# Performance work log

Measured on AMD Instinct MI355X. Metric: run time of the kernel, lower is better.

The kernel has to match this reference:

```python
import jax, jax.numpy as jnp
import numpy as np

K = 9      # kernel_size
H = 6      # num_head
HD = 64    # head_dim
D = H * HD # reduced_hidden_dim = 384
B, S = 16, 1024
OUT = 384  # hidden_dim // 2


def setup_inputs() -> dict:
    key = jax.random.key(0)
    k = jax.random.split(key, 5)
    q = jax.random.normal(k[0], (B, S, D), dtype=jnp.float32)
    ks = jax.random.normal(k[1], (B, S, D), dtype=jnp.float32)
    v = jax.random.normal(k[2], (B, S, D), dtype=jnp.float32)
    Wk = jax.random.normal(k[3], (K * H, D), dtype=jnp.float32) * 0.02
    bk = jnp.zeros((K * H,), dtype=jnp.float32)
    Wp = jax.random.normal(k[4], (OUT, D), dtype=jnp.float32) * 0.02
    bp = jnp.zeros((OUT,), dtype=jnp.float32)
    return {"q": q, "ks": ks, "v": v, "Wk": Wk, "bk": bk, "Wp": Wp, "bp": bp}


def reference(q, ks, v, Wk, bk, Wp, bp):
    b, s, d = v.shape
    pad = K // 2
    # expand4conv: zero-pad along seq and gather K-wide sliding windows
    vp = jnp.pad(v, ((0, 0), (pad, pad), (0, 0)))            # [B, S+K-1, D]
    win = jnp.stack([vp[:, i:i + s] for i in range(K)], -1)  # [B, S, D, K]
    win = win.reshape(b, s, H, HD, K)                        # [B, S, H, HD, K]
    # dynamic kernel: softmax over kernel taps
    logits = jnp.einsum('bsd,od->bso', q * ks, Wk) + bk       # [B, S, K*H]
    dk = jax.nn.softmax(logits.reshape(b, s, H, K), axis=-1)  # [B, S, H, K]
    # local weighted reduction over the window
    out = jnp.einsum('bshdk,bshk->bshd', win, dk).reshape(b, s, d)
    return jnp.einsum('bsd,od->bso', out, Wp) + bp            # [B, S, OUT]
```

## Files before the change

### kernel.cpp

```cpp
#include <hip/hip_runtime.h>
#include <hip/hip_bf16.h>

#define BB 16
#define SS 1024
#define DD 384
#define HH 6
#define KK 9
#define KH 54
#define OUTD 384
#define NKT 12
#define VLD 392
#define RPB 32
#define NTH 512

typedef __attribute__((ext_vector_type(4))) float floatx4;
typedef __attribute__((ext_vector_type(8))) __bf16 bf16x8;
typedef __attribute__((ext_vector_type(4))) __bf16 bf16x4;

__global__ __launch_bounds__(256) void cast_kernel(const float* __restrict__ Wk,
                                                   const float* __restrict__ Wp,
                                                   __bf16* __restrict__ WkT,
                                                   __bf16* __restrict__ WpT) {
    int i = blockIdx.x * 256 + threadIdx.x;
    if (i < 4 * NKT * 64 * 8) {
        int e = i & 7, lane = (i >> 3) & 63, t = i >> 9;
        int kstep = t % NKT, ntile = t / NKT;
        int row = ntile * 16 + (lane & 15);
        int col = kstep * 32 + ((lane >> 4) << 3) + e;
        WkT[i] = (row < KH) ? (__bf16)Wk[row * DD + col] : (__bf16)0.0f;
    } else if (i < 24576 + 24 * NKT * 64 * 8) {
        int j = i - 24576;
        int e = j & 7, lane = (j >> 3) & 63, t = j >> 9;
        int kstep = t % NKT, ntile = t / NKT;
        int row = ntile * 16 + (lane & 15);
        int col = kstep * 32 + ((lane >> 4) << 3) + e;
        WpT[j] = (__bf16)Wp[row * DD + col];
    }
}

__global__ __launch_bounds__(NTH, 8) void fused_kernel(const float* __restrict__ q,
                                                       const float* __restrict__ ks,
                                                       const float* __restrict__ v,
                                                       const __bf16* __restrict__ WkT,
                                                       const float* __restrict__ bk,
                                                       const __bf16* __restrict__ WpT,
                                                       const float* __restrict__ bp,
                                                       float* __restrict__ out) {
    __shared__ __bf16 vS[40 * VLD];
    __shared__ float  lgS[RPB * 66];

    const int tid  = threadIdx.x;
    const int wave = tid >> 6;
    const int lane = tid & 63;
    const int m0   = blockIdx.x * RPB;
    const int b    = blockIdx.x >> 5;
    const int s0   = (blockIdx.x & 31) * RPB;
    const int fr   = lane & 15;
    const int fk   = (lane >> 4) * 8;
    const int col_in = lane & 15;
    const int rgrp   = (lane >> 4) * 4;

    {
        const float* vb = v + (size_t)b * SS * DD;
#pragma unroll
        for (int it = 0; it < 8; ++it) {
            int c = tid + it * NTH;
            if (c < 3840) {
                int row = c / 96, col = (c % 96) * 4;
                int r = s0 + row - 4;
                int rc = r < 0 ? 0 : (r > SS - 1 ? SS - 1 : r);
                floatx4 val = *reinterpret_cast<const floatx4*>(vb + (size_t)rc * DD + col);
                if (r < 0 || r >= SS) val = floatx4{0.0f, 0.0f, 0.0f, 0.0f};
                bf16x4 vk4 = { (__bf16)val.x, (__bf16)val.y, (__bf16)val.z, (__bf16)val.w };
                *reinterpret_cast<bf16x4*>(&vS[row * VLD + col]) = vk4;
            }
        }
    }

    {
        const int rt = wave >> 2;
        const int nt = wave & 3;
        const float* qrow = q  + (size_t)(m0 + rt * 16 + fr) * DD + fk;
        const float* krow = ks + (size_t)(m0 + rt * 16 + fr) * DD + fk;
        const __bf16* wkb = WkT + (((nt * NKT) * 64 + lane) << 3);
        bf16x8 wf0 = *reinterpret_cast<const bf16x8*>(wkb);
        bf16x8 wf1;
        floatx4 acc = {};
#pragma unroll
        for (int s = 0; s < NKT; ++s) {
            if (s + 1 < NKT) {
                const __bf16* nb = wkb + ((size_t)(s + 1) << 9);
                if ((s & 1) == 0) wf1 = *reinterpret_cast<const bf16x8*>(nb);
                else              wf0 = *reinterpret_cast<const bf16x8*>(nb);
            }
            floatx4 q0 = *reinterpret_cast<const floatx4*>(qrow + s * 32);
            floatx4 q1 = *reinterpret_cast<const floatx4*>(qrow + s * 32 + 4);
            floatx4 k0 = *reinterpret_cast<const floatx4*>(krow + s * 32);
            floatx4 k1 = *reinterpret_cast<const floatx4*>(krow + s * 32 + 4);
            floatx4 p0 = q0 * k0, p1 = q1 * k1;
            bf16x8 af = { (__bf16)p0.x, (__bf16)p0.y, (__bf16)p0.z, (__bf16)p0.w,
                          (__bf16)p1.x, (__bf16)p1.y, (__bf16)p1.z, (__bf16)p1.w };
            acc = __builtin_amdgcn_mfma_f32_16x16x32_bf16(
                af, (s & 1) == 0 ? wf0 : wf1, acc, 0, 0, 0);
        }
#pragma unroll
        for (int r = 0; r < 4; ++r)
            lgS[(rt * 16 + rgrp + r) * 66 + nt * 16 + col_in] = acc[r];
    }
    __syncthreads();

    if (tid < RPB * HH) {
        int row = tid / HH, h = tid % HH;
        float lg[KK];
        float mx = -1e30f;
#pragma unroll
        for (int k = 0; k < KK; ++k) {
            float s = lgS[row * 66 + h * KK + k] + bk[h * KK + k];
            lg[k] = s;
            mx = fmaxf(mx, s);
        }
        float sum = 0.0f;
#pragma unroll
        for (int k = 0; k < KK; ++k) { lg[k] = __expf(lg[k] - mx); sum += lg[k]; }
        float inv = 1.0f / sum;
#pragma unroll
        for (int k = 0; k < KK; ++k) lgS[row * 66 + h * KK + k] = lg[k] * inv;
    }
    __syncthreads();

    bf16x4 aR[6];
#pragma unroll
    for (int it = 0; it < 6; ++it) {
        int p = tid + it * NTH;
        int row = p / 96, c4 = p % 96;
        int h = c4 >> 4;
        const float* dkr = &lgS[row * 66 + h * KK];
        floatx4 a = {};
#pragma unroll
        for (int k = 0; k < KK; ++k) {
            bf16x4 w = *reinterpret_cast<const bf16x4*>(&vS[(row + k) * VLD + c4 * 4]);
            floatx4 wf = { (float)w[0], (float)w[1], (float)w[2], (float)w[3] };
            a += wf * dkr[k];
        }
        aR[it] = bf16x4{ (__bf16)a.x, (__bf16)a.y, (__bf16)a.z, (__bf16)a.w };
    }

    const int nt0 = wave * 3;
    const __bf16* wpb = WpT + (((nt0 * NKT) * 64 + lane) << 3);
    bf16x8 bfr[2][3];
#pragma unroll
    for (int j = 0; j < 3; ++j)
        bfr[0][j] = *reinterpret_cast<const bf16x8*>(wpb + ((size_t)(j * NKT) << 9));

    __syncthreads();

#pragma unroll
    for (int it = 0; it < 6; ++it) {
        int p = tid + it * NTH;
        int row = p / 96, c4 = p % 96;
        *reinterpret_cast<bf16x4*>(&vS[row * VLD + c4 * 4]) = aR[it];
    }
    __syncthreads();

    {
        floatx4 acc[2][3] = {};
#pragma unroll
        for (int s = 0; s < NKT; ++s) {
            const int cur = s & 1, nxt = cur ^ 1;
            if (s + 1 < NKT) {
#pragma unroll
                for (int j = 0; j < 3; ++j)
                    bfr[nxt][j] = *reinterpret_cast<const bf16x8*>(
                        wpb + ((size_t)(j * NKT + s + 1) << 9));
            }
            bf16x8 a0 = *reinterpret_cast<const bf16x8*>(&vS[fr * VLD + s * 32 + fk]);
            bf16x8 a1 = *reinterpret_cast<const bf16x8*>(&vS[(16 + fr) * VLD + s * 32 + fk]);
#pragma unroll
            for (int j = 0; j < 3; ++j) {
                acc[0][j] = __builtin_amdgcn_mfma_f32_16x16x32_bf16(a0, bfr[cur][j], acc[0][j], 0, 0, 0);
                acc[1][j] = __builtin_amdgcn_mfma_f32_16x16x32_bf16(a1, bfr[cur][j], acc[1][j], 0, 0, 0);
            }
        }
        float* ob = out + (size_t)m0 * OUTD;
#pragma unroll
        for (int j = 0; j < 3; ++j) {
            int col = (nt0 + j) * 16 + col_in;
            float bv = bp[col];
#pragma unroll
            for (int rt = 0; rt < 2; ++rt)
#pragma unroll
                for (int r = 0; r < 4; ++r)
                    ob[(size_t)(rt * 16 + rgrp + r) * OUTD + col] = acc[rt][j][r] + bv;
        }
    }
}

extern "C" void kernel_launch(void* const* d_in, const int* in_sizes, int n_in,
                              void* d_out, int out_size, void* d_ws, size_t ws_size,
                              hipStream_t stream) {
    const float* q  = (const float*)d_in[0];
    const float* ks = (const float*)d_in[1];
    const float* v  = (const float*)d_in[2];
    const float* Wk = (const float*)d_in[3];
    const float* bk = (const float*)d_in[4];
    const float* Wp = (const float*)d_in[5];
    const float* bp = (const float*)d_in[6];
    float* out = (float*)d_out;

    __bf16* WkT = (__bf16*)d_ws;
    __bf16* WpT = (__bf16*)((char*)d_ws + 49152);

    cast_kernel<<<(24576 + 147456 + 255) / 256, 256, 0, stream>>>(Wk, Wp, WkT, WpT);
    fused_kernel<<<(BB * SS) / RPB, NTH, 0, stream>>>(q, ks, v, WkT, bk, WpT, bp, out);
}
```

Baseline: 141.4 us.

## Split fused kernel into conv kernel writing MFMA-layout A and separate projection GEMM

After: 147.7 us. 1.04x slower.

```diff
diff --git a/kernel.cpp b/kernel.cpp
--- a/kernel.cpp
+++ b/kernel.cpp
@@ -10,8 +10,6 @@
 #define OUTD 384
 #define NKT 12
 #define VLD 392
-#define RPB 32
-#define NTH 512
 
 typedef __attribute__((ext_vector_type(4))) float floatx4;
 typedef __attribute__((ext_vector_type(8))) __bf16 bf16x8;
@@ -38,51 +36,31 @@
     }
 }
 
-__global__ __launch_bounds__(NTH, 8) void fused_kernel(const float* __restrict__ q,
+__global__ __launch_bounds__(256, 4) void convA_kernel(const float* __restrict__ q,
                                                        const float* __restrict__ ks,
                                                        const float* __restrict__ v,
                                                        const __bf16* __restrict__ WkT,
                                                        const float* __restrict__ bk,
-                                                       const __bf16* __restrict__ WpT,
-                                                       const float* __restrict__ bp,
-                                                       float* __restrict__ out) {
-    __shared__ __bf16 vS[40 * VLD];
-    __shared__ float  lgS[RPB * 66];
+                                                       __bf16* __restrict__ A) {
+    __shared__ __bf16 vS[24 * VLD];
+    __shared__ float  lgS[16 * 66];
 
     const int tid  = threadIdx.x;
     const int wave = tid >> 6;
     const int lane = tid & 63;
-    const int m0   = blockIdx.x * RPB;
-    const int b    = blockIdx.x >> 5;
-    const int s0   = (blockIdx.x & 31) * RPB;
+    const int mt   = blockIdx.x;
+    const int m0   = mt * 16;
+    const int b    = mt >> 6;
+    const int s0   = (mt & 63) * 16;
     const int fr   = lane & 15;
     const int fk   = (lane >> 4) * 8;
     const int col_in = lane & 15;
     const int rgrp   = (lane >> 4) * 4;
 
     {
-        const float* vb = v + (size_t)b * SS * DD;
-#pragma unroll
-        for (int it = 0; it < 8; ++it) {
-            int c = tid + it * NTH;
-            if (c < 3840) {
-                int row = c / 96, col = (c % 96) * 4;
-                int r = s0 + row - 4;
-                int rc = r < 0 ? 0 : (r > SS - 1 ? SS - 1 : r);
-                floatx4 val = *reinterpret_cast<const floatx4*>(vb + (size_t)rc * DD + col);
-                if (r < 0 || r >= SS) val = floatx4{0.0f, 0.0f, 0.0f, 0.0f};
-                bf16x4 vk4 = { (__bf16)val.x, (__bf16)val.y, (__bf16)val.z, (__bf16)val.w };
-                *reinterpret_cast<bf16x4*>(&vS[row * VLD + col]) = vk4;
-            }
-        }
-    }
-
-    {
-        const int rt = wave >> 2;
-        const int nt = wave & 3;
-        const float* qrow = q  + (size_t)(m0 + rt * 16 + fr) * DD + fk;
-        const float* krow = ks + (size_t)(m0 + rt * 16 + fr) * DD + fk;
-        const __bf16* wkb = WkT + (((nt * NKT) * 64 + lane) << 3);
+        const float* qrow = q  + (size_t)(m0 + fr) * DD + fk;
+        const float* krow = ks + (size_t)(m0 + fr) * DD + fk;
+        const __bf16* wkb = WkT + (((wave * NKT) * 64 + lane) << 3);
         bf16x8 wf0 = *reinterpret_cast<const bf16x8*>(wkb);
         bf16x8 wf1;
         floatx4 acc = {};
@@ -105,11 +83,22 @@
         }
 #pragma unroll
         for (int r = 0; r < 4; ++r)
-            lgS[(rt * 16 + rgrp + r) * 66 + nt * 16 + col_in] = acc[r];
+            lgS[(rgrp + r) * 66 + wave * 16 + col_in] = acc[r];
+    }
+
+    floatx4 vpre[9];
+#pragma unroll
+    for (int it = 0; it < 9; ++it) {
+        int c = tid + it * 256;
+        int row = c / 96, col = (c % 96) * 4;
+        int r = s0 + row - 4;
+        int rc = r < 0 ? 0 : (r > SS - 1 ? SS - 1 : r);
+        vpre[it] = *reinterpret_cast<const floatx4*>(
+            v + (size_t)b * SS * DD + (size_t)rc * DD + col);
     }
     __syncthreads();
 
-    if (tid < RPB * HH) {
+    if (tid < 16 * HH) {
         int row = tid / HH, h = tid % HH;
         float lg[KK];
         float mx = -1e30f;
@@ -126,12 +115,22 @@
 #pragma unroll
         for (int k = 0; k < KK; ++k) lgS[row * 66 + h * KK + k] = lg[k] * inv;
     }
+
+#pragma unroll
+    for (int it = 0; it < 9; ++it) {
+        int c = tid + it * 256;
+        int row = c / 96, col = (c % 96) * 4;
+        int r = s0 + row - 4;
+        floatx4 val = vpre[it];
+        if (r < 0 || r >= SS) val = floatx4{0.0f, 0.0f, 0.0f, 0.0f};
+        bf16x4 vk4 = { (__bf16)val.x, (__bf16)val.y, (__bf16)val.z, (__bf16)val.w };
+        *reinterpret_cast<bf16x4*>(&vS[row * VLD + col]) = vk4;
+    }
     __syncthreads();
 
-    bf16x4 aR[6];
 #pragma unroll
     for (int it = 0; it < 6; ++it) {
-        int p = tid + it * NTH;
+        int p = tid + it * 256;
         int row = p / 96, c4 = p % 96;
         int h = c4 >> 4;
         const float* dkr = &lgS[row * 66 + h * KK];
@@ -142,56 +141,66 @@
             floatx4 wf = { (float)w[0], (float)w[1], (float)w[2], (float)w[3] };
             a += wf * dkr[k];
         }
-        aR[it] = bf16x4{ (__bf16)a.x, (__bf16)a.y, (__bf16)a.z, (__bf16)a.w };
-    }
-
-    const int nt0 = wave * 3;
-    const __bf16* wpb = WpT + (((nt0 * NKT) * 64 + lane) << 3);
-    bf16x8 bfr[2][3];
+        int cb = c4 * 4;
+        int s = cb >> 5, kq = (cb >> 3) & 3, e0 = cb & 7;
+        bf16x4 o = { (__bf16)a.x, (__bf16)a.y, (__bf16)a.z, (__bf16)a.w };
+        *reinterpret_cast<bf16x4*>(
+            A + ((((size_t)mt * NKT + s) * 64 + (row + 16 * kq)) << 3) + e0) = o;
+    }
+}
+
+__global__ __launch_bounds__(512, 4) void gemmB_kernel(const __bf16* __restrict__ A,
+                                                       const __bf16* __restrict__ WpT,
+                                                       const float* __restrict__ bp,
+                                                       float* __restrict__ out) {
+    const int tid  = threadIdx.x;
+    const int wave = tid >> 6;
+    const int lane = tid & 63;
+    const int m0   = blockIdx.x * 32;
+    const int mt0  = blockIdx.x * 2;
+    const int nt0  = wave * 3;
+    const int col_in = lane & 15;
+    const int rgrp   = (lane >> 4) * 4;
+
+    const __bf16* a0b = A + ((((size_t)mt0     * NKT) * 64 + lane) << 3);
+    const __bf16* a1b = A + ((((size_t)(mt0+1) * NKT) * 64 + lane) << 3);
+    const __bf16* wpb = WpT + ((((size_t)nt0 * NKT) * 64 + lane) << 3);
+
+    bf16x8 af[2][2], bfr[2][3];
+    af[0][0] = *reinterpret_cast<const bf16x8*>(a0b);
+    af[0][1] = *reinterpret_cast<const bf16x8*>(a1b);
 #pragma unroll
     for (int j = 0; j < 3; ++j)
         bfr[0][j] = *reinterpret_cast<const bf16x8*>(wpb + ((size_t)(j * NKT) << 9));
 
-    __syncthreads();
-
-#pragma unroll
-    for (int it = 0; it < 6; ++it) {
-        int p = tid + it * NTH;
-        int row = p / 96, c4 = p % 96;
-        *reinterpret_cast<bf16x4*>(&vS[row * VLD + c4 * 4]) = aR[it];
-    }
-    __syncthreads();
-
-    {
-        floatx4 acc[2][3] = {};
-#pragma unroll
-        for (int s = 0; s < NKT; ++s) {
-            const int cur = s & 1, nxt = cur ^ 1;
-            if (s + 1 < NKT) {
-#pragma unroll
-                for (int j = 0; j < 3; ++j)
-                    bfr[nxt][j] = *reinterpret_cast<const bf16x8*>(
-                        wpb + ((size_t)(j * NKT + s + 1) << 9));
-            }
-            bf16x8 a0 = *reinterpret_cast<const bf16x8*>(&vS[fr * VLD + s * 32 + fk]);
-            bf16x8 a1 = *reinterpret_cast<const bf16x8*>(&vS[(16 + fr) * VLD + s * 32 + fk]);
-#pragma unroll
-            for (int j = 0; j < 3; ++j) {
-                acc[0][j] = __builtin_amdgcn_mfma_f32_16x16x32_bf16(a0, bfr[cur][j], acc[0][j], 0, 0, 0);
-                acc[1][j] = __builtin_amdgcn_mfma_f32_16x16x32_bf16(a1, bfr[cur][j], acc[1][j], 0, 0, 0);
-            }
-        }
-        float* ob = out + (size_t)m0 * OUTD;
+    floatx4 acc[2][3] = {};
+#pragma unroll
+    for (int s = 0; s < NKT; ++s) {
+        const int cur = s & 1, nxt = cur ^ 1;
+        if (s + 1 < NKT) {
+            af[nxt][0] = *reinterpret_cast<const bf16x8*>(a0b + ((size_t)(s + 1) << 9));
+            af[nxt][1] = *reinterpret_cast<const bf16x8*>(a1b + ((size_t)(s + 1) << 9));
+#pragma unroll
+            for (int j = 0; j < 3; ++j)
+                bfr[nxt][j] = *reinterpret_cast<const bf16x8*>(
+                    wpb + ((size_t)(j * NKT + s + 1) << 9));
+        }
 #pragma unroll
         for (int j = 0; j < 3; ++j) {
-            int col = (nt0 + j) * 16 + col_in;
-            float bv = bp[col];
-#pragma unroll
-            for (int rt = 0; rt < 2; ++rt)
-#pragma unroll
-                for (int r = 0; r < 4; ++r)
-                    ob[(size_t)(rt * 16 + rgrp + r) * OUTD + col] = acc[rt][j][r] + bv;
-        }
+            acc[0][j] = __builtin_amdgcn_mfma_f32_16x16x32_bf16(af[cur][0], bfr[cur][j], acc[0][j], 0, 0, 0);
+            acc[1][j] = __builtin_amdgcn_mfma_f32_16x16x32_bf16(af[cur][1], bfr[cur][j], acc[1][j], 0, 0, 0);
+        }
+    }
+    float* ob = out + (size_t)m0 * OUTD;
+#pragma unroll
+    for (int j = 0; j < 3; ++j) {
+        int col = (nt0 + j) * 16 + col_in;
+        float bv = bp[col];
+#pragma unroll
+        for (int rt = 0; rt < 2; ++rt)
+#pragma unroll
+            for (int r = 0; r < 4; ++r)
+                ob[(size_t)(rt * 16 + rgrp + r) * OUTD + col] = acc[rt][j][r] + bv;
     }
 }
 
@@ -209,7 +218,9 @@
 
     __bf16* WkT = (__bf16*)d_ws;
     __bf16* WpT = (__bf16*)((char*)d_ws + 49152);
+    __bf16* A   = (__bf16*)((char*)d_ws + 49152 + 294912);
 
     cast_kernel<<<(24576 + 147456 + 255) / 256, 256, 0, stream>>>(Wk, Wp, WkT, WpT);
-    fused_kernel<<<(BB * SS) / RPB, NTH, 0, stream>>>(q, ks, v, WkT, bk, WpT, bp, out);
-}
+    convA_kernel<<<BB * SS / 16, 256, 0, stream>>>(q, ks, v, WkT, bk, A);
+    gemmB_kernel<<<BB * SS / 32, 512, 0, stream>>>(A, WpT, bp, out);
+}
```
